# Kernel tuning notes

Hardware: AMD Instinct MI355X
Metric: run time of the kernel (lower is better)

The kernel has to match this reference:

```python
import jax, jax.numpy as jnp
import numpy as np

STRIDE = 4; R = 3; LEVELS = 4; LAT = 128; RES = (384, 512); D_IN = 1110; T_EMB = 50

def _sincos_1d(d, pos):
    omega = np.arange(d // 2, dtype=np.float64) / (d / 2.0)
    omega = 1.0 / 10000 ** omega
    out = pos.reshape(-1)[:, None] * omega[None, :]
    return np.concatenate([np.sin(out), np.cos(out)], axis=1).astype(np.float32)

def _support(coords, r):
    # coords [B, N, 3] (t, x, y) -> [B, N, 2r+1, 2r+1, 3]; offsets only in x,y
    d = jnp.linspace(-r, r, 2 * r + 1, dtype=jnp.float32)
    g0, g1 = jnp.meshgrid(d, d, indexing='ij')
    delta = jnp.stack([jnp.zeros_like(g0), g0, g1], axis=-1)
    return coords[:, :, None, None, :] + delta[None, None]

def _trilinear(fmap, coords):
    # fmap [B, C, Dd, H, W]; coords [B, M, 3] = (t, x, y); border padding, align_corners=True
    B, C, Dd, H, W = fmap.shape
    t = jnp.clip(coords[..., 0], 0.0, Dd - 1)
    x = jnp.clip(coords[..., 1], 0.0, W - 1)
    y = jnp.clip(coords[..., 2], 0.0, H - 1)
    t0f = jnp.floor(t); x0f = jnp.floor(x); y0f = jnp.floor(y)
    wt = (t - t0f)[:, None, :]; wx = (x - x0f)[:, None, :]; wy = (y - y0f)[:, None, :]
    t0 = t0f.astype(jnp.int32); t1 = jnp.minimum(t0 + 1, Dd - 1)
    x0 = x0f.astype(jnp.int32); x1 = jnp.minimum(x0 + 1, W - 1)
    y0 = y0f.astype(jnp.int32); y1 = jnp.minimum(y0 + 1, H - 1)
    flat = fmap.reshape(B, C, Dd * H * W)
    def g(ti, yi, xi):
        idx = (ti * H + yi) * W + xi
        return jnp.take_along_axis(flat, idx[:, None, :], axis=2)  # [B, C, M]
    def bilin(ti):
        v00 = g(ti, y0, x0); v01 = g(ti, y0, x1); v10 = g(ti, y1, x0); v11 = g(ti, y1, x1)
        return (v00 * (1 - wy) * (1 - wx) + v01 * (1 - wy) * wx
                + v10 * wy * (1 - wx) + v11 * wy * wx)
    return bilin(t0) * (1 - wt) + bilin(t1) * wt

def _posenc(x, min_deg, max_deg):
    scales = 2.0 ** jnp.arange(min_deg, max_deg, dtype=jnp.float32)
    xb = (x[..., None, :] * scales[:, None]).reshape(x.shape[:-1] + (-1,))
    ff = jnp.sin(jnp.concatenate([xb, xb + 0.5 * jnp.pi], axis=-1))
    return jnp.concatenate([x, ff], axis=-1)

def _interp_time(emb, t):
    T0 = emb.shape[1]
    if t == T0:
        return emb
    sc = T0 / float(t)
    j = jnp.clip((jnp.arange(t, dtype=jnp.float32) + 0.5) * sc - 0.5, 0.0, T0 - 1)
    j0 = jnp.floor(j).astype(jnp.int32); j1 = jnp.minimum(j0 + 1, T0 - 1)
    w = (j - j0)[None, :, None]
    return emb[:, j0] * (1 - w) + emb[:, j1] * w

def setup_inputs():
    key = jax.random.key(0)
    ks = jax.random.split(key, 10)
    B, T, N, H, W = 1, 16, 128, RES[0], RES[1]
    video = jax.random.uniform(ks[0], (B, T, 3, H, W), jnp.float32) * 255.0
    fr = jax.random.randint(ks[1], (B, N), 0, T).astype(jnp.float32)
    cx = jax.random.uniform(ks[2], (B, N), jnp.float32) * (W - 1)
    cy = jax.random.uniform(ks[3], (B, N), jnp.float32) * (H - 1)
    queries = jnp.stack([fr, cx, cy], axis=-1)
    s = 0.02
    return {
        'video': video,
        'queries': queries,
        'fnet_w': jax.random.normal(ks[4], (LAT, 3, 4, 4), jnp.float32) * s,
        'fnet_b': jnp.zeros((LAT,), jnp.float32),
        'fc1_w': jax.random.normal(ks[5], (2401, 384), jnp.float32) * s,
        'fc1_b': jnp.zeros((384,), jnp.float32),
        'fc2_w': jax.random.normal(ks[6], (384, 256), jnp.float32) * s,
        'fc2_b': jnp.zeros((256,), jnp.float32),
        'up_w1': jax.random.normal(ks[7], (D_IN, 384), jnp.float32) * s,
        'up_b1': jnp.zeros((384,), jnp.float32),
        'up_w2': jax.random.normal(ks[8], (384, 4), jnp.float32) * s,
        'up_b2': jnp.zeros((4,), jnp.float32),
        'time_emb': jnp.asarray(_sincos_1d(D_IN, np.linspace(0, T_EMB - 1, T_EMB))[None]),
        'iters': 4,
    }

def reference(video, queries, fnet_w, fnet_b, fc1_w, fc1_b, fc2_w, fc2_b,
              up_w1, up_b1, up_w2, up_b2, time_emb, iters):
    B, T, C, H, W = video.shape
    N = queries.shape[1]
    video = 2.0 * (video / 255.0) - 1.0
    qf = queries[:, :, 0]            # queried frames (used as float t coordinate)
    qc = queries[..., 1:3] / STRIDE  # (x, y) in feature-map coords
    # --- encoder (stand-in conv), L2-normalize over channels ---
    f = jax.lax.conv_general_dilated(video.reshape(B * T, C, H, W), fnet_w,
                                     (STRIDE, STRIDE), 'VALID') + fnet_b[None, :, None, None]
    f = f / jnp.sqrt(jnp.maximum(jnp.sum(f * f, axis=1, keepdims=True), 1e-12))
    fmaps = f.reshape(B, T, LAT, H // STRIDE, W // STRIDE)
    # --- avg-pool pyramid ---
    pyr = [fmaps]
    for _ in range(LEVELS - 1):
        p = pyr[-1]
        pyr.append(p.reshape(B, T, LAT, p.shape[-2] // 2, 2, p.shape[-1] // 2, 2).mean(axis=(4, 6)))
    r = R; rr = 2 * r + 1
    # --- track support features per level: [B, N, rr, rr, LAT] ---
    tfs = []
    for i in range(LEVELS):
        sc = jnp.concatenate([qf[..., None], qc / (2.0 ** i)], axis=-1)  # [B,N,3]
        sp = _support(sc, r).reshape(B, N * rr * rr, 3)
        feat = _trilinear(pyr[i].transpose(0, 2, 1, 3, 4), sp)  # [B, LAT, N*rr*rr]
        tfs.append(feat.reshape(B, LAT, N, rr, rr).transpose(0, 2, 3, 4, 1))
    vis = jnp.zeros((B, T, N), jnp.float32)
    conf = jnp.zeros((B, T, N), jnp.float32)
    coords = jnp.broadcast_to(qc.reshape(B, 1, N, 2), (B, T, N, 2)).astype(jnp.float32)
    scale = jnp.array([RES[1], RES[0]], jnp.float32) / STRIDE
    te = _interp_time(time_emb, T)  # [1, T, D_IN]
    for _ in range(iters):
        coords = jax.lax.stop_gradient(coords)
        cflat = coords.reshape(B * T, N, 2)
        embs = []
        for i in range(LEVELS):
            fm = pyr[i]
            Hi, Wi = fm.shape[-2], fm.shape[-1]
            sc = jnp.concatenate([jnp.zeros_like(cflat[..., :1]), cflat / (2.0 ** i)], axis=-1)
            sp = _support(sc, r).reshape(B * T, N * rr * rr, 3)
            cf = _trilinear(fm.reshape(B * T, LAT, 1, Hi, Wi), sp)  # [B*T, LAT, N*rr*rr]
            cf = cf.reshape(B, T, LAT, N, rr, rr).transpose(0, 1, 3, 4, 5, 2)  # [B,T,N,rr,rr,LAT]
            cv = jnp.einsum('btnhwc,bnijc->btnhwij', cf, tfs[i]).reshape(B * T * N, rr * rr * rr * rr)
            e = jax.nn.gelu(cv @ fc1_w + fc1_b, approximate=False) @ fc2_w + fc2_b
            embs.append(e)
        corr = jnp.concatenate(embs, axis=-1).reshape(B, T, N, -1)  # [B,T,N,1024]
        rf = jnp.pad(coords[:, :-1] - coords[:, 1:], ((0, 0), (0, 1), (0, 0), (0, 0))) / scale
        rb = jnp.pad(coords[:, 1:] - coords[:, :-1], ((0, 0), (1, 0), (0, 0), (0, 0))) / scale
        pe = _posenc(jnp.concatenate([rf, rb], axis=-1), 0, 10)  # [B,T,N,84]
        x = jnp.concatenate([vis[..., None], conf[..., None], corr, pe], axis=-1)  # [B,T,N,1110]
        x = x.transpose(0, 2, 1, 3) + te[None]  # [B,N,T,1110]
        delta = jax.nn.gelu(x @ up_w1 + up_b1, approximate=False) @ up_w2 + up_b2  # [B,N,T,4]
        coords = coords + delta[..., :2].transpose(0, 2, 1, 3)
        vis = vis + delta[..., 2].transpose(0, 2, 1)
        conf = conf + delta[..., 3].transpose(0, 2, 1)
    return coords * float(STRIDE), jax.nn.sigmoid(vis), jax.nn.sigmoid(conf)
```

## Files before the change

### kernel.cpp

```cpp
#include <hip/hip_runtime.h>
#include <math.h>

#define T_FR   16
#define N_Q    128
#define NSUP   49
#define H0     96
#define W0     128
#define DIN    1110
#define ITERS  4
#define KCV    2560
#define KU     1152

typedef __attribute__((ext_vector_type(8))) short short8;
typedef __attribute__((ext_vector_type(4))) float f32x4;

__device__ __forceinline__ float geluf(float x) {
    return 0.5f * x * (1.0f + erff(x * 0.70710678118654752f));
}
__device__ __forceinline__ unsigned short f2bf(float f) {
    unsigned u = __float_as_uint(f);
    u += 0x7fff + ((u >> 16) & 1);
    return (unsigned short)(u >> 16);
}
__device__ __forceinline__ float bf2f(unsigned short s) {
    return __uint_as_float(((unsigned)s) << 16);
}
__device__ __forceinline__ void async16(const void* g, void* l) {
    __builtin_amdgcn_global_load_lds(
        (const __attribute__((address_space(1))) void*)g,
        (__attribute__((address_space(3))) void*)l, 16, 0, 0);
}

__global__ void k_te(const float* __restrict__ emb, float* __restrict__ te) {
    int i = blockIdx.x * 256 + threadIdx.x;
    if (i >= T_FR * DIN) return;
    int t = i / DIN, d = i - t * DIN;
    float j = ((float)t + 0.5f) * (50.0f / 16.0f) - 0.5f;
    j = fminf(fmaxf(j, 0.0f), 49.0f);
    float j0f = floorf(j);
    int j0 = (int)j0f;
    int j1 = min(j0 + 1, 49);
    float w = j - j0f;
    te[i] = emb[j0 * DIN + d] * (1.0f - w) + emb[j1 * DIN + d] * w;
}

__global__ void k_init(const float* __restrict__ q, float* __restrict__ coords,
                       float* __restrict__ vis, float* __restrict__ conf) {
    int r = blockIdx.x * 256 + threadIdx.x;
    if (r >= T_FR * N_Q) return;
    int n = r & 127;
    coords[r * 2 + 0] = q[n * 3 + 1] * 0.25f;
    coords[r * 2 + 1] = q[n * 3 + 2] * 0.25f;
    vis[r] = 0.0f;
    conf[r] = 0.0f;
}

__global__ void k_prep1(const float* __restrict__ w, unsigned short* __restrict__ wt) {
    int i = blockIdx.x * 256 + threadIdx.x;
    if (i >= 2401 * 384) return;
    int k = i / 384, n = i - k * 384;
    int p = k / 49, q = k - p * 49;
    wt[(size_t)n * KCV + q * 52 + p] = f2bf(w[i]);
}

__global__ void k_prep(const float* __restrict__ w, unsigned short* __restrict__ wt,
                       int K, int N, int Ka, int total) {
    int i = blockIdx.x * 256 + threadIdx.x;
    if (i >= total) return;
    int k = i / N, n = i - k * N;
    wt[(size_t)n * Ka + k] = f2bf(w[i]);
}

__global__ void k_prepc(const float* __restrict__ w, unsigned short* __restrict__ wc) {
    int i = blockIdx.x * 256 + threadIdx.x;
    if (i >= 128 * 64) return;
    int ch = i >> 6, k = i & 63;
    wc[i] = (k < 48) ? f2bf(w[ch * 48 + k]) : (unsigned short)0;
}

#define APAD 72
__global__ __launch_bounds__(256) void k_conv(const float* __restrict__ video,
                                              const unsigned short* __restrict__ wc,
                                              const float* __restrict__ b,
                                              unsigned short* __restrict__ out) {
    __shared__ __align__(16) short As[128 * APAD];
    __shared__ __align__(16) short Bs[128 * APAD];
    const int y = blockIdx.x;
    const int tf = blockIdx.y;
    const int tid = threadIdx.x;

    {
        int pos = tid >> 1, half = tid & 1;
        short8 z = (short8){0,0,0,0,0,0,0,0};
        *(short8*)&As[pos * APAD + 48 + half * 8] = z;
    }
    #pragma unroll
    for (int s = 0; s < 6; ++s) {
        int chunk = s * 256 + tid;
        int c = chunk >> 9, r = chunk & 511;
        int ky = r >> 7, pos = r & 127;
        float4 v = *(const float4*)&video[(((size_t)(tf * 3 + c) * 384) + 4 * y + ky) * 512 + pos * 4];
        unsigned short o[4];
        o[0] = f2bf(v.x * (2.0f / 255.0f) - 1.0f);
        o[1] = f2bf(v.y * (2.0f / 255.0f) - 1.0f);
        o[2] = f2bf(v.z * (2.0f / 255.0f) - 1.0f);
        o[3] = f2bf(v.w * (2.0f / 255.0f) - 1.0f);
        *(uint2*)&As[pos * APAD + c * 16 + ky * 4] = *(const uint2*)o;
    }
    #pragma unroll
    for (int s = 0; s < 4; ++s) {
        int chunk = s * 256 + tid;
        int row = chunk >> 3, q = chunk & 7;
        *(uint4*)&Bs[row * APAD + q * 8] = *(const uint4*)&wc[row * 64 + q * 8];
    }
    __syncthreads();

    const int w = tid >> 6, lane = tid & 63, ml = lane & 15, quad = lane >> 4;
    f32x4 acc[2][8];
    #pragma unroll
    for (int mi = 0; mi < 2; ++mi)
        #pragma unroll
        for (int ni = 0; ni < 8; ++ni) acc[mi][ni] = (f32x4){0.f, 0.f, 0.f, 0.f};
    #pragma unroll
    for (int kk = 0; kk < 2; ++kk) {
        short8 af[2];
        #pragma unroll
        for (int mi = 0; mi < 2; ++mi)
            af[mi] = *(const short8*)&As[(w * 32 + mi * 16 + ml) * APAD + kk * 32 + quad * 8];
        #pragma unroll
        for (int ni = 0; ni < 8; ++ni) {
            short8 bv = *(const short8*)&Bs[(ni * 16 + ml) * APAD + kk * 32 + quad * 8];
            #pragma unroll
            for (int mi = 0; mi < 2; ++mi)
                acc[mi][ni] = __builtin_amdgcn_mfma_f32_16x16x32_bf16(af[mi], bv, acc[mi][ni], 0, 0, 0);
        }
    }
    float bias[8];
    #pragma unroll
    for (int ni = 0; ni < 8; ++ni) bias[ni] = b[ni * 16 + ml];
    unsigned short* obase = out + ((size_t)(tf * 96 + y) * 128) * 128;
    #pragma unroll
    for (int mi = 0; mi < 2; ++mi) {
        float s2[4];
        #pragma unroll
        for (int reg = 0; reg < 4; ++reg) {
            float s = 0.f;
            #pragma unroll
            for (int ni = 0; ni < 8; ++ni) {
                float v = acc[mi][ni][reg] + bias[ni];
                s = fmaf(v, v, s);
            }
            s += __shfl_xor(s, 1); s += __shfl_xor(s, 2);
            s += __shfl_xor(s, 4); s += __shfl_xor(s, 8);
            s2[reg] = rsqrtf(fmaxf(s, 1e-12f));
        }
        #pragma unroll
        for (int reg = 0; reg < 4; ++reg) {
            int pos = w * 32 + mi * 16 + quad * 4 + reg;
            #pragma unroll
            for (int ni = 0; ni < 8; ++ni)
                obase[(size_t)pos * 128 + ni * 16 + ml] = f2bf((acc[mi][ni][reg] + bias[ni]) * s2[reg]);
        }
    }
}

__global__ void k_pool(const unsigned short* __restrict__ in, unsigned short* __restrict__ out,
                       int Ho, int Wo, int total8) {
    int i = blockIdx.x * 256 + threadIdx.x;
    if (i >= total8) return;
    int c8 = i & 15;
    int rest = i >> 4;
    int x = rest % Wo; rest /= Wo;
    int y = rest % Ho;
    int bt = rest / Ho;
    int Wi = Wo * 2;
    const unsigned short* base = in + (size_t)bt * (Ho * 2) * Wi * 128;
    const unsigned short* p00 = base + ((size_t)(2 * y) * Wi + 2 * x) * 128 + c8 * 8;
    const unsigned short* p10 = base + ((size_t)(2 * y + 1) * Wi + 2 * x) * 128 + c8 * 8;
    unsigned short o[8];
    #pragma unroll
    for (int k = 0; k < 8; ++k)
        o[k] = f2bf(0.25f * (bf2f(p00[k]) + bf2f(p00[128 + k]) + bf2f(p10[k]) + bf2f(p10[128 + k])));
    unsigned short* dst = out + (size_t)i * 8;
    *(uint4*)dst = *(const uint4*)o;
}

__global__ __launch_bounds__(256) void k_template(const float* __restrict__ q,
    const unsigned short* __restrict__ p0, const unsigned short* __restrict__ p1,
    const unsigned short* __restrict__ p2, const unsigned short* __restrict__ p3,
    unsigned short* __restrict__ tfs) {
    __shared__ float gw[NSUP * 4];
    __shared__ int go[NSUP * 4];
    const int lvl = blockIdx.x >> 7;
    const int n = blockIdx.x & 127;
    const int tid = threadIdx.x;
    const unsigned short* fm; int Hi, Wi;
    if (lvl == 0)      { fm = p0; Hi = 96; Wi = 128; }
    else if (lvl == 1) { fm = p1; Hi = 48; Wi = 64; }
    else if (lvl == 2) { fm = p2; Hi = 24; Wi = 32; }
    else               { fm = p3; Hi = 12; Wi = 16; }
    float t = fminf(fmaxf(q[n * 3 + 0], 0.0f), (float)(T_FR - 1));
    float t0f = floorf(t);
    float wt = t - t0f;
    int t0 = (int)t0f, t1 = min(t0 + 1, T_FR - 1);
    if (tid < NSUP) {
        float inv = 1.0f / (float)(1 << lvl);
        float x = fminf(fmaxf(q[n * 3 + 1] * 0.25f * inv + (float)(tid / 7 - 3), 0.0f), (float)(Wi - 1));
        float y = fminf(fmaxf(q[n * 3 + 2] * 0.25f * inv + (float)(tid % 7 - 3), 0.0f), (float)(Hi - 1));
        float x0f = floorf(x), y0f = floorf(y);
        float wx = x - x0f, wy = y - y0f;
        int x0 = (int)x0f, y0 = (int)y0f;
        int x1 = min(x0 + 1, Wi - 1), y1 = min(y0 + 1, Hi - 1);
        gw[tid * 4 + 0] = (1 - wy) * (1 - wx);
        gw[tid * 4 + 1] = (1 - wy) * wx;
        gw[tid * 4 + 2] = wy * (1 - wx);
        gw[tid * 4 + 3] = wy * wx;
        go[tid * 4 + 0] = (y0 * Wi + x0) * 128;
        go[tid * 4 + 1] = (y0 * Wi + x1) * 128;
        go[tid * 4 + 2] = (y1 * Wi + x0) * 128;
        go[tid * 4 + 3] = (y1 * Wi + x1) * 128;
    }
    __syncthreads();
    size_t fs = (size_t)Hi * Wi * 128;
    const unsigned short* f0 = fm + (size_t)t0 * fs;
    const unsigned short* f1 = fm + (size_t)t1 * fs;
    unsigned short* obase = tfs + ((size_t)lvl * N_Q + n) * 64 * 128;
    #pragma unroll
    for (int s = 0; s < 4; ++s) {
        int i = s * 256 + tid;
        int p = i >> 4, c8 = i & 15;
        unsigned short o[8];
        if (p >= NSUP) {
            uint4 z = {0, 0, 0, 0};
            *(uint4*)&obase[(size_t)p * 128 + c8 * 8] = z;
            continue;
        }
        int o0 = go[p * 4 + 0] + c8 * 8, o1 = go[p * 4 + 1] + c8 * 8;
        int o2 = go[p * 4 + 2] + c8 * 8, o3 = go[p * 4 + 3] + c8 * 8;
        float w0 = gw[p * 4 + 0], w1 = gw[p * 4 + 1], w2 = gw[p * 4 + 2], w3 = gw[p * 4 + 3];
        uint4 a0 = *(const uint4*)&f0[o0], a1 = *(const uint4*)&f0[o1];
        uint4 a2 = *(const uint4*)&f0[o2], a3 = *(const uint4*)&f0[o3];
        uint4 b0 = *(const uint4*)&f1[o0], b1 = *(const uint4*)&f1[o1];
        uint4 b2 = *(const uint4*)&f1[o2], b3 = *(const uint4*)&f1[o3];
        const unsigned short* s0 = (const unsigned short*)&a0;
        const unsigned short* s1 = (const unsigned short*)&a1;
        const unsigned short* s2 = (const unsigned short*)&a2;
        const unsigned short* s3 = (const unsigned short*)&a3;
        const unsigned short* r0 = (const unsigned short*)&b0;
        const unsigned short* r1 = (const unsigned short*)&b1;
        const unsigned short* r2 = (const unsigned short*)&b2;
        const unsigned short* r3 = (const unsigned short*)&b3;
        #pragma unroll
        for (int j = 0; j < 8; ++j) {
            float v0 = w0 * bf2f(s0[j]) + w1 * bf2f(s1[j]) + w2 * bf2f(s2[j]) + w3 * bf2f(s3[j]);
            float v1 = w0 * bf2f(r0[j]) + w1 * bf2f(r1[j]) + w2 * bf2f(r2[j]) + w3 * bf2f(r3[j]);
            o[j] = f2bf(v0 * (1 - wt) + v1 * wt);
        }
        *(uint4*)&obase[(size_t)p * 128 + c8 * 8] = *(const uint4*)o;
    }
}

#define CPAD 136
__global__ __launch_bounds__(256) void k_corr(
    const unsigned short* __restrict__ p0, const unsigned short* __restrict__ p1,
    const unsigned short* __restrict__ p2, const unsigned short* __restrict__ p3,
    const unsigned short* __restrict__ tfs, const float* __restrict__ coords,
    unsigned short* __restrict__ cv) {
    __shared__ __align__(16) short tf_s[64 * CPAD];
    __shared__ __align__(16) short cf_s[64 * CPAD];
    __shared__ float gw[NSUP * 4];
    __shared__ int go[NSUP * 4];
    const int id = blockIdx.x;
    const int xcd = id & 7;
    const int j = id >> 3;
    const int lvl = j >> 8;
    const int bt = ((j >> 7) & 1) * 8 + xcd;
    const int n = j & 127;
    const int r = lvl * 2048 + bt * 128 + n;
    const int tid = threadIdx.x;

    const unsigned short* tsrc = tfs + ((size_t)lvl * N_Q + n) * 64 * 128;
    #pragma unroll
    for (int s = 0; s < 4; ++s) {
        int ch = s * 256 + tid;
        int row = ch >> 4, c8 = ch & 15;
        *(uint4*)&tf_s[row * CPAD + c8 * 8] = *(const uint4*)&tsrc[row * 128 + c8 * 8];
    }
    if (tid < 240) {
        int row = NSUP + tid / 16, c8 = tid % 16;
        uint4 z = {0, 0, 0, 0};
        *(uint4*)&cf_s[row * CPAD + c8 * 8] = z;
    }

    const unsigned short* fm; int Hi, Wi;
    if (lvl == 0)      { fm = p0; Hi = 96; Wi = 128; }
    else if (lvl == 1) { fm = p1; Hi = 48; Wi = 64; }
    else if (lvl == 2) { fm = p2; Hi = 24; Wi = 32; }
    else               { fm = p3; Hi = 12; Wi = 16; }
    if (tid < NSUP) {
        float inv = 1.0f / (float)(1 << lvl);
        float cx = coords[((size_t)bt * N_Q + n) * 2 + 0] * inv;
        float cy = coords[((size_t)bt * N_Q + n) * 2 + 1] * inv;
        float x = fminf(fmaxf(cx + (float)(tid / 7 - 3), 0.0f), (float)(Wi - 1));
        float y = fminf(fmaxf(cy + (float)(tid % 7 - 3), 0.0f), (float)(Hi - 1));
        float x0f = floorf(x), y0f = floorf(y);
        float wx = x - x0f, wy = y - y0f;
        int x0 = (int)x0f, y0 = (int)y0f;
        int x1 = min(x0 + 1, Wi - 1), y1 = min(y0 + 1, Hi - 1);
        gw[tid * 4 + 0] = (1 - wy) * (1 - wx);
        gw[tid * 4 + 1] = (1 - wy) * wx;
        gw[tid * 4 + 2] = wy * (1 - wx);
        gw[tid * 4 + 3] = wy * wx;
        go[tid * 4 + 0] = (y0 * Wi + x0) * 128;
        go[tid * 4 + 1] = (y0 * Wi + x1) * 128;
        go[tid * 4 + 2] = (y1 * Wi + x0) * 128;
        go[tid * 4 + 3] = (y1 * Wi + x1) * 128;
    }
    __syncthreads();

    const unsigned short* fbase = fm + (size_t)bt * Hi * Wi * 128;
    for (int i = tid; i < NSUP * 16; i += 256) {
        int p = i >> 4, c8 = i & 15;
        int o0 = go[p * 4 + 0] + c8 * 8, o1 = go[p * 4 + 1] + c8 * 8;
        int o2 = go[p * 4 + 2] + c8 * 8, o3 = go[p * 4 + 3] + c8 * 8;
        float w0 = gw[p * 4 + 0], w1 = gw[p * 4 + 1], w2 = gw[p * 4 + 2], w3 = gw[p * 4 + 3];
        uint4 a0 = *(const uint4*)&fbase[o0], a1 = *(const uint4*)&fbase[o1];
        uint4 a2 = *(const uint4*)&fbase[o2], a3 = *(const uint4*)&fbase[o3];
        const unsigned short* s0 = (const unsigned short*)&a0;
        const unsigned short* s1 = (const unsigned short*)&a1;
        const unsigned short* s2 = (const unsigned short*)&a2;
        const unsigned short* s3 = (const unsigned short*)&a3;
        unsigned short o[8];
        #pragma unroll
        for (int jj = 0; jj < 8; ++jj)
            o[jj] = f2bf(w0 * bf2f(s0[jj]) + w1 * bf2f(s1[jj]) + w2 * bf2f(s2[jj]) + w3 * bf2f(s3[jj]));
        *(uint4*)&cf_s[p * CPAD + c8 * 8] = *(const uint4*)o;
    }
    __syncthreads();

    const int w = tid >> 6, lane = tid & 63, ml = lane & 15, quad = lane >> 4;
    f32x4 acc[4];
    #pragma unroll
    for (int ni = 0; ni < 4; ++ni) acc[ni] = (f32x4){0.f, 0.f, 0.f, 0.f};
    #pragma unroll
    for (int kk = 0; kk < 4; ++kk) {
        short8 a = *(const short8*)&cf_s[(w * 16 + ml) * CPAD + kk * 32 + quad * 8];
        #pragma unroll
        for (int ni = 0; ni < 4; ++ni) {
            short8 b = *(const short8*)&tf_s[(ni * 16 + ml) * CPAD + kk * 32 + quad * 8];
            acc[ni] = __builtin_amdgcn_mfma_f32_16x16x32_bf16(a, b, acc[ni], 0, 0, 0);
        }
    }
    unsigned short* crow = cv + (size_t)r * KCV;
    const int p_base = w * 16 + quad * 4;
    #pragma unroll
    for (int ni = 0; ni < 4; ++ni) {
        int q = ni * 16 + ml;
        if (q < NSUP && p_base < 52) {
            unsigned short o4[4];
            #pragma unroll
            for (int reg = 0; reg < 4; ++reg) o4[reg] = f2bf(acc[ni][reg]);
            *(uint2*)&crow[q * 52 + p_base] = *(const uint2*)o4;
        }
    }
    if (tid < 12) crow[2548 + tid] = 0;
}

__global__ __launch_bounds__(256) void k_fc1(const unsigned short* __restrict__ A,
                                             const unsigned short* __restrict__ Wt,
                                             const float* __restrict__ bias,
                                             unsigned short* __restrict__ C,
                                             int Ka, int nbn, int nbm, int ldc) {
    __shared__ __align__(16) short As[64 * 32];
    __shared__ __align__(16) short Bs[128 * 32];
    const int id = blockIdx.x;
    const int xcd = id & 7;
    const int j = id >> 3;
    const int mpx = nbm >> 3;
    const int m_blk = xcd * mpx + j / nbn;
    const int n_blk = j % nbn;
    const int gm0 = m_blk * 64, n0 = n_blk * 128;
    const int tid = threadIdx.x;
    const int w = tid >> 6, lane = tid & 63, ml = lane & 15, quad = lane >> 4;
    const int wm = w >> 1, wn = w & 1;
    const int wbase = (tid & 192) * 16;
    f32x4 acc[2][4];
    #pragma unroll
    for (int mi = 0; mi < 2; ++mi)
        #pragma unroll
        for (int ni = 0; ni < 4; ++ni) acc[mi][ni] = (f32x4){0.f, 0.f, 0.f, 0.f};
    const unsigned short* gA = A + (size_t)(gm0 + (tid >> 2)) * Ka + (tid & 3) * 8;
    const unsigned short* gB = Wt + (size_t)n0 * Ka;
    for (int k0 = 0; k0 < Ka; k0 += 32) {
        async16(gA + k0, (char*)As + wbase);
        #pragma unroll
        for (int s = 0; s < 2; ++s) {
            int chunk = s * 256 + tid;
            int m = chunk >> 2, q = chunk & 3;
            async16(gB + (size_t)m * Ka + k0 + q * 8, (char*)Bs + s * 4096 + wbase);
        }
        __syncthreads();
        short8 af[2], bfr[4];
        #pragma unroll
        for (int mi = 0; mi < 2; ++mi)
            af[mi] = *(const short8*)&As[(wm * 32 + mi * 16 + ml) * 32 + quad * 8];
        #pragma unroll
        for (int ni = 0; ni < 4; ++ni)
            bfr[ni] = *(const short8*)&Bs[(wn * 64 + ni * 16 + ml) * 32 + quad * 8];
        #pragma unroll
        for (int mi = 0; mi < 2; ++mi)
            #pragma unroll
            for (int ni = 0; ni < 4; ++ni)
                acc[mi][ni] = __builtin_amdgcn_mfma_f32_16x16x32_bf16(af[mi], bfr[ni], acc[mi][ni], 0, 0, 0);
        __syncthreads();
    }
    #pragma unroll
    for (int mi = 0; mi < 2; ++mi) {
        #pragma unroll
        for (int ni = 0; ni < 4; ++ni) {
            int gn = n0 + wn * 64 + ni * 16 + ml;
            float bv = bias[gn];
            #pragma unroll
            for (int reg = 0; reg < 4; ++reg) {
                int gm = gm0 + wm * 32 + mi * 16 + quad * 4 + reg;
                C[(size_t)gm * ldc + gn] = f2bf(geluf(acc[mi][ni][reg] + bv));
            }
        }
    }
}

__global__ __launch_bounds__(256) void k_mgemm64(const unsigned short* __restrict__ A,
                                                 const unsigned short* __restrict__ Wt,
                                                 const float* __restrict__ bias,
                                                 void* __restrict__ Cout,
                                                 const float* __restrict__ te,
                                                 int Ka, int nbn, int nbm, int ldc, int mode) {
    __shared__ __align__(16) short As[64 * 64];
    __shared__ __align__(16) short Bs[64 * 64];
    const int id = blockIdx.x;
    const int xcd = id & 7;
    const int j = id >> 3;
    const int mpx = nbm >> 3;
    const int m_blk = xcd * mpx + j / nbn;
    const int n_blk = j % nbn;
    const int gm0 = m_blk * 64, n0 = n_blk * 64;
    const int tid = threadIdx.x;
    const int w = tid >> 6, lane = tid & 63, ml = lane & 15, quad = lane >> 4;
    const int wm = w >> 1, wn = w & 1;
    const int wbase = (tid & 192) * 16;
    const int srow = tid >> 3, sq = tid & 7;
    f32x4 acc[2][2];
    #pragma unroll
    for (int mi = 0; mi < 2; ++mi)
        #pragma unroll
        for (int ni = 0; ni < 2; ++ni) acc[mi][ni] = (f32x4){0.f, 0.f, 0.f, 0.f};
    const unsigned short* gA = A + (size_t)(gm0 + srow) * Ka + sq * 8;
    const unsigned short* gB = Wt + (size_t)(n0 + srow) * Ka + sq * 8;
    for (int k0 = 0; k0 < Ka; k0 += 64) {
        async16(gA + k0,           (char*)As + wbase);
        async16(gA + 32 * Ka + k0, (char*)As + 4096 + wbase);
        async16(gB + k0,           (char*)Bs + wbase);
        async16(gB + 32 * Ka + k0, (char*)Bs + 4096 + wbase);
        __syncthreads();
        #pragma unroll
        for (int kk = 0; kk < 2; ++kk) {
            short8 af[2], bfr[2];
            #pragma unroll
            for (int mi = 0; mi < 2; ++mi)
                af[mi] = *(const short8*)&As[(wm * 32 + mi * 16 + ml) * 64 + kk * 32 + quad * 8];
            #pragma unroll
            for (int ni = 0; ni < 2; ++ni)
                bfr[ni] = *(const short8*)&Bs[(wn * 32 + ni * 16 + ml) * 64 + kk * 32 + quad * 8];
            #pragma unroll
            for (int mi = 0; mi < 2; ++mi)
                #pragma unroll
                for (int ni = 0; ni < 2; ++ni)
                    acc[mi][ni] = __builtin_amdgcn_mfma_f32_16x16x32_bf16(af[mi], bfr[ni], acc[mi][ni], 0, 0, 0);
        }
        __syncthreads();
    }
    #pragma unroll
    for (int mi = 0; mi < 2; ++mi) {
        #pragma unroll
        for (int ni = 0; ni < 2; ++ni) {
            int gn = n0 + wn * 32 + ni * 16 + ml;
            float bv = bias[gn];
            #pragma unroll
            for (int reg = 0; reg < 4; ++reg) {
                int gm = gm0 + wm * 32 + mi * 16 + quad * 4 + reg;
                float v = acc[mi][ni][reg] + bv;
                if (mode == 1) v = geluf(v);
                if (mode == 2) {
                    int row = gm & 2047, lvl = gm >> 11;
                    int d = 2 + lvl * 256 + gn;
                    int t = row >> 7;
                    ((unsigned short*)Cout)[(size_t)row * KU + d] = f2bf(v + te[t * DIN + d]);
                } else {
                    ((unsigned short*)Cout)[(size_t)gm * ldc + gn] = f2bf(v);
                }
            }
        }
    }
}

__global__ __launch_bounds__(128) void k_assemble(const float* __restrict__ coords,
                           const float* __restrict__ vis, const float* __restrict__ conf,
                           const float* __restrict__ te, unsigned short* __restrict__ x) {
    int r = blockIdx.x;
    int tid = threadIdx.x;
    int d = (tid < 2) ? tid : 1024 + tid;
    int t = r >> 7, n = r & 127;
    if (d >= DIN) { x[(size_t)r * KU + d] = 0; return; }
    float v;
    if (d == 0) v = vis[r];
    else if (d == 1) v = conf[r];
    else {
        int dd = d - 1026;
        float c0x = coords[r * 2], c0y = coords[r * 2 + 1];
        float v4[4];
        if (t < T_FR - 1) {
            v4[0] = (c0x - coords[((t + 1) * N_Q + n) * 2 + 0]) * (1.0f / 128.0f);
            v4[1] = (c0y - coords[((t + 1) * N_Q + n) * 2 + 1]) * (1.0f / 96.0f);
        } else { v4[0] = 0.f; v4[1] = 0.f; }
        if (t > 0) {
            v4[2] = (c0x - coords[((t - 1) * N_Q + n) * 2 + 0]) * (1.0f / 128.0f);
            v4[3] = (c0y - coords[((t - 1) * N_Q + n) * 2 + 1]) * (1.0f / 96.0f);
        } else { v4[2] = 0.f; v4[3] = 0.f; }
        if (dd < 4) v = v4[dd];
        else if (dd < 44) { int s = (dd - 4) >> 2, k = (dd - 4) & 3; v = sinf(v4[k] * (float)(1 << s)); }
        else              { int s = (dd - 44) >> 2, k = (dd - 44) & 3; v = cosf(v4[k] * (float)(1 << s)); }
    }
    x[(size_t)r * KU + d] = f2bf(v + te[t * DIN + d]);
}

__global__ __launch_bounds__(256) void k_up2(const unsigned short* __restrict__ h1,
                                             const float* __restrict__ w2,
                                             const float* __restrict__ b2,
                                             float* __restrict__ coords,
                                             float* __restrict__ vis,
                                             float* __restrict__ conf) {
    const int w = threadIdx.x >> 6, lane = threadIdx.x & 63;
    const int r = blockIdx.x * 4 + w;
    float a0 = 0.f, a1 = 0.f, a2 = 0.f, a3 = 0.f;
    if (lane < 48) {
        short8 av = *(const short8*)&h1[(size_t)r * 384 + lane * 8];
        const float* wp = w2 + lane * 32;
        #pragma unroll
        for (int j = 0; j < 8; ++j) {
            float x = bf2f((unsigned short)av[j]);
            a0 = fmaf(x, wp[j * 4 + 0], a0);
            a1 = fmaf(x, wp[j * 4 + 1], a1);
            a2 = fmaf(x, wp[j * 4 + 2], a2);
            a3 = fmaf(x, wp[j * 4 + 3], a3);
        }
    }
    #pragma unroll
    for (int m = 32; m > 0; m >>= 1) {
        a0 += __shfl_xor(a0, m); a1 += __shfl_xor(a1, m);
        a2 += __shfl_xor(a2, m); a3 += __shfl_xor(a3, m);
    }
    if (lane == 0) {
        coords[r * 2 + 0] += a0 + b2[0];
        coords[r * 2 + 1] += a1 + b2[1];
        vis[r] += a2 + b2[2];
        conf[r] += a3 + b2[3];
    }
}

__global__ void k_output(const float* __restrict__ coords, const float* __restrict__ vis,
                         const float* __restrict__ conf, float* __restrict__ out) {
    int r = blockIdx.x * 256 + threadIdx.x;
    if (r >= T_FR * N_Q) return;
    out[r * 2 + 0] = coords[r * 2 + 0] * 4.0f;
    out[r * 2 + 1] = coords[r * 2 + 1] * 4.0f;
    out[4096 + r] = 1.0f / (1.0f + expf(-vis[r]));
    out[6144 + r] = 1.0f / (1.0f + expf(-conf[r]));
}

extern "C" void kernel_launch(void* const* d_in, const int* in_sizes, int n_in,
                              void* d_out, int out_size, void* d_ws, size_t ws_size,
                              hipStream_t stream) {
    const float* video   = (const float*)d_in[0];
    const float* queries = (const float*)d_in[1];
    const float* fnet_w  = (const float*)d_in[2];
    const float* fnet_b  = (const float*)d_in[3];
    const float* fc1_w   = (const float*)d_in[4];
    const float* fc1_b   = (const float*)d_in[5];
    const float* fc2_w   = (const float*)d_in[6];
    const float* fc2_b   = (const float*)d_in[7];
    const float* up_w1   = (const float*)d_in[8];
    const float* up_b1   = (const float*)d_in[9];
    const float* up_w2   = (const float*)d_in[10];
    const float* up_b2   = (const float*)d_in[11];
    const float* t_emb   = (const float*)d_in[12];

    char* wsb = (char*)d_ws;
    size_t off = 0;
    #define ALLOC_US(name, elems) unsigned short* name = (unsigned short*)(wsb + off); off += ((size_t)(elems) * 2 + 15) & ~15ull;
    #define ALLOC_F(name, elems)  float* name = (float*)(wsb + off); off += ((size_t)(elems) * 4 + 15) & ~15ull;
    ALLOC_US(pyr0, (size_t)16 * 96 * 128 * 128)
    ALLOC_US(pyr1, (size_t)16 * 48 * 64 * 128)
    ALLOC_US(pyr2, (size_t)16 * 24 * 32 * 128)
    ALLOC_US(pyr3, (size_t)16 * 12 * 16 * 128)
    ALLOC_US(tfs,  (size_t)4 * N_Q * 64 * 128)
    ALLOC_US(cv,   (size_t)8192 * KCV)
    ALLOC_US(h1,   (size_t)8192 * 384)
    ALLOC_US(xb,   (size_t)2048 * KU)
    ALLOC_US(wt1,  (size_t)384 * KCV)
    ALLOC_US(wt2,  (size_t)256 * 384)
    ALLOC_US(wtu,  (size_t)384 * KU)
    ALLOC_US(wcv,  (size_t)128 * 64)
    ALLOC_F(te,   (size_t)T_FR * DIN)
    ALLOC_F(crd,  (size_t)2048 * 2)
    ALLOC_F(vis,  2048)
    ALLOC_F(conf, 2048)

    k_te<<<(T_FR * DIN + 255) / 256, 256, 0, stream>>>(t_emb, te);
    k_init<<<8, 256, 0, stream>>>(queries, crd, vis, conf);
    hipMemsetAsync(wt1, 0, (size_t)384 * KCV * 2, stream);
    k_prep1<<<(2401 * 384 + 255) / 256, 256, 0, stream>>>(fc1_w, wt1);
    k_prep<<<(384 * 256 + 255) / 256, 256, 0, stream>>>(fc2_w, wt2, 384, 256, 384, 384 * 256);
    k_prep<<<(DIN * 384 + 255) / 256, 256, 0, stream>>>(up_w1, wtu, DIN, 384, KU, DIN * 384);
    k_prepc<<<32, 256, 0, stream>>>(fnet_w, wcv);
    k_conv<<<dim3(96, 16), 256, 0, stream>>>(video, wcv, fnet_b, pyr0);
    k_pool<<<(16 * 48 * 64 * 16 + 255) / 256, 256, 0, stream>>>(pyr0, pyr1, 48, 64, 16 * 48 * 64 * 16);
    k_pool<<<(16 * 24 * 32 * 16 + 255) / 256, 256, 0, stream>>>(pyr1, pyr2, 24, 32, 16 * 24 * 32 * 16);
    k_pool<<<(16 * 12 * 16 * 16 + 255) / 256, 256, 0, stream>>>(pyr2, pyr3, 12, 16, 16 * 12 * 16 * 16);
    k_template<<<4 * N_Q, 256, 0, stream>>>(queries, pyr0, pyr1, pyr2, pyr3, tfs);

    for (int it = 0; it < ITERS; ++it) {
        k_corr<<<8192, 256, 0, stream>>>(pyr0, pyr1, pyr2, pyr3, tfs, crd, cv);
        k_fc1<<<384, 256, 0, stream>>>(cv, wt1, fc1_b, h1, KCV, 3, 128, 384);
        k_assemble<<<2048, 128, 0, stream>>>(crd, vis, conf, te, xb);
        k_mgemm64<<<512, 256, 0, stream>>>(h1, wt2, fc2_b, xb, te, 384, 4, 128, 0, 2);
        k_mgemm64<<<192, 256, 0, stream>>>(xb, wtu, up_b1, h1, nullptr, KU, 6, 32, 384, 1);
        k_up2<<<512, 256, 0, stream>>>(h1, up_w2, up_b2, crd, vis, conf);
    }
    k_output<<<8, 256, 0, stream>>>(crd, vis, conf, (float*)d_out);
}
```

Before: 649.1 us.

## Replace LDS-staged GEMMs with register-prefetched direct-global-load MFMA kernel

Measured after the change: 930.5 us. 43.3% more time.

```diff
diff --git a/kernel.cpp b/kernel.cpp
--- a/kernel.cpp
+++ b/kernel.cpp
@@ -366,77 +366,12 @@
     if (tid < 12) crow[2548 + tid] = 0;
 }
 
-__global__ __launch_bounds__(256) void k_fc1(const unsigned short* __restrict__ A,
-                                             const unsigned short* __restrict__ Wt,
-                                             const float* __restrict__ bias,
-                                             unsigned short* __restrict__ C,
-                                             int Ka, int nbn, int nbm, int ldc) {
-    __shared__ __align__(16) short As[64 * 32];
-    __shared__ __align__(16) short Bs[128 * 32];
-    const int id = blockIdx.x;
-    const int xcd = id & 7;
-    const int j = id >> 3;
-    const int mpx = nbm >> 3;
-    const int m_blk = xcd * mpx + j / nbn;
-    const int n_blk = j % nbn;
-    const int gm0 = m_blk * 64, n0 = n_blk * 128;
-    const int tid = threadIdx.x;
-    const int w = tid >> 6, lane = tid & 63, ml = lane & 15, quad = lane >> 4;
-    const int wm = w >> 1, wn = w & 1;
-    const int wbase = (tid & 192) * 16;
-    f32x4 acc[2][4];
-    #pragma unroll
-    for (int mi = 0; mi < 2; ++mi)
-        #pragma unroll
-        for (int ni = 0; ni < 4; ++ni) acc[mi][ni] = (f32x4){0.f, 0.f, 0.f, 0.f};
-    const unsigned short* gA = A + (size_t)(gm0 + (tid >> 2)) * Ka + (tid & 3) * 8;
-    const unsigned short* gB = Wt + (size_t)n0 * Ka;
-    for (int k0 = 0; k0 < Ka; k0 += 32) {
-        async16(gA + k0, (char*)As + wbase);
-        #pragma unroll
-        for (int s = 0; s < 2; ++s) {
-            int chunk = s * 256 + tid;
-            int m = chunk >> 2, q = chunk & 3;
-            async16(gB + (size_t)m * Ka + k0 + q * 8, (char*)Bs + s * 4096 + wbase);
-        }
-        __syncthreads();
-        short8 af[2], bfr[4];
-        #pragma unroll
-        for (int mi = 0; mi < 2; ++mi)
-            af[mi] = *(const short8*)&As[(wm * 32 + mi * 16 + ml) * 32 + quad * 8];
-        #pragma unroll
-        for (int ni = 0; ni < 4; ++ni)
-            bfr[ni] = *(const short8*)&Bs[(wn * 64 + ni * 16 + ml) * 32 + quad * 8];
-        #pragma unroll
-        for (int mi = 0; mi < 2; ++mi)
-            #pragma unroll
-            for (int ni = 0; ni < 4; ++ni)
-                acc[mi][ni] = __builtin_amdgcn_mfma_f32_16x16x32_bf16(af[mi], bfr[ni], acc[mi][ni], 0, 0, 0);
-        __syncthreads();
-    }
-    #pragma unroll
-    for (int mi = 0; mi < 2; ++mi) {
-        #pragma unroll
-        for (int ni = 0; ni < 4; ++ni) {
-            int gn = n0 + wn * 64 + ni * 16 + ml;
-            float bv = bias[gn];
-            #pragma unroll
-            for (int reg = 0; reg < 4; ++reg) {
-                int gm = gm0 + wm * 32 + mi * 16 + quad * 4 + reg;
-                C[(size_t)gm * ldc + gn] = f2bf(geluf(acc[mi][ni][reg] + bv));
-            }
-        }
-    }
-}
-
-__global__ __launch_bounds__(256) void k_mgemm64(const unsigned short* __restrict__ A,
-                                                 const unsigned short* __restrict__ Wt,
-                                                 const float* __restrict__ bias,
-                                                 void* __restrict__ Cout,
-                                                 const float* __restrict__ te,
-                                                 int Ka, int nbn, int nbm, int ldc, int mode) {
-    __shared__ __align__(16) short As[64 * 64];
-    __shared__ __align__(16) short Bs[64 * 64];
+__global__ __launch_bounds__(256) void k_greg(const unsigned short* __restrict__ A,
+                                              const unsigned short* __restrict__ Wt,
+                                              const float* __restrict__ bias,
+                                              void* __restrict__ Cout,
+                                              const float* __restrict__ te,
+                                              int Ka, int nbn, int nbm, int ldc, int mode) {
     const int id = blockIdx.x;
     const int xcd = id & 7;
     const int j = id >> 3;
@@ -447,38 +382,56 @@
     const int tid = threadIdx.x;
     const int w = tid >> 6, lane = tid & 63, ml = lane & 15, quad = lane >> 4;
     const int wm = w >> 1, wn = w & 1;
-    const int wbase = (tid & 192) * 16;
-    const int srow = tid >> 3, sq = tid & 7;
+
     f32x4 acc[2][2];
     #pragma unroll
     for (int mi = 0; mi < 2; ++mi)
         #pragma unroll
         for (int ni = 0; ni < 2; ++ni) acc[mi][ni] = (f32x4){0.f, 0.f, 0.f, 0.f};
-    const unsigned short* gA = A + (size_t)(gm0 + srow) * Ka + sq * 8;
-    const unsigned short* gB = Wt + (size_t)(n0 + srow) * Ka + sq * 8;
-    for (int k0 = 0; k0 < Ka; k0 += 64) {
-        async16(gA + k0,           (char*)As + wbase);
-        async16(gA + 32 * Ka + k0, (char*)As + 4096 + wbase);
-        async16(gB + k0,           (char*)Bs + wbase);
-        async16(gB + 32 * Ka + k0, (char*)Bs + 4096 + wbase);
-        __syncthreads();
+
+    const unsigned short* pa0 = A + (size_t)(gm0 + wm * 32 + ml) * Ka + quad * 8;
+    const unsigned short* pa1 = pa0 + (size_t)16 * Ka;
+    const unsigned short* pb0 = Wt + (size_t)(n0 + wn * 32 + ml) * Ka + quad * 8;
+    const unsigned short* pb1 = pb0 + (size_t)16 * Ka;
+
+    short8 a0[2][2], b0[2][2];
+    #pragma unroll
+    for (int kk = 0; kk < 2; ++kk) {
+        a0[0][kk] = *(const short8*)(pa0 + kk * 32);
+        a0[1][kk] = *(const short8*)(pa1 + kk * 32);
+        b0[0][kk] = *(const short8*)(pb0 + kk * 32);
+        b0[1][kk] = *(const short8*)(pb1 + kk * 32);
+    }
+    for (int k0 = 64; k0 < Ka; k0 += 64) {
+        short8 a1[2][2], b1[2][2];
         #pragma unroll
         for (int kk = 0; kk < 2; ++kk) {
-            short8 af[2], bfr[2];
-            #pragma unroll
-            for (int mi = 0; mi < 2; ++mi)
-                af[mi] = *(const short8*)&As[(wm * 32 + mi * 16 + ml) * 64 + kk * 32 + quad * 8];
-            #pragma unroll
-            for (int ni = 0; ni < 2; ++ni)
-                bfr[ni] = *(const short8*)&Bs[(wn * 32 + ni * 16 + ml) * 64 + kk * 32 + quad * 8];
+            a1[0][kk] = *(const short8*)(pa0 + k0 + kk * 32);
+            a1[1][kk] = *(const short8*)(pa1 + k0 + kk * 32);
+            b1[0][kk] = *(const short8*)(pb0 + k0 + kk * 32);
+            b1[1][kk] = *(const short8*)(pb1 + k0 + kk * 32);
+        }
+        #pragma unroll
+        for (int kk = 0; kk < 2; ++kk)
             #pragma unroll
             for (int mi = 0; mi < 2; ++mi)
                 #pragma unroll
                 for (int ni = 0; ni < 2; ++ni)
-                    acc[mi][ni] = __builtin_amdgcn_mfma_f32_16x16x32_bf16(af[mi], bfr[ni], acc[mi][ni], 0, 0, 0);
-        }
-        __syncthreads();
-    }
+                    acc[mi][ni] = __builtin_amdgcn_mfma_f32_16x16x32_bf16(a0[mi][kk], b0[ni][kk], acc[mi][ni], 0, 0, 0);
+        #pragma unroll
+        for (int kk = 0; kk < 2; ++kk) {
+            a0[0][kk] = a1[0][kk]; a0[1][kk] = a1[1][kk];
+            b0[0][kk] = b1[0][kk]; b0[1][kk] = b1[1][kk];
+        }
+    }
+    #pragma unroll
+    for (int kk = 0; kk < 2; ++kk)
+        #pragma unroll
+        for (int mi = 0; mi < 2; ++mi)
+            #pragma unroll
+            for (int ni = 0; ni < 2; ++ni)
+                acc[mi][ni] = __builtin_amdgcn_mfma_f32_16x16x32_bf16(a0[mi][kk], b0[ni][kk], acc[mi][ni], 0, 0, 0);
+
     #pragma unroll
     for (int mi = 0; mi < 2; ++mi) {
         #pragma unroll
@@ -630,10 +583,10 @@
 
     for (int it = 0; it < ITERS; ++it) {
         k_corr<<<8192, 256, 0, stream>>>(pyr0, pyr1, pyr2, pyr3, tfs, crd, cv);
-        k_fc1<<<384, 256, 0, stream>>>(cv, wt1, fc1_b, h1, KCV, 3, 128, 384);
+        k_greg<<<768, 256, 0, stream>>>(cv, wt1, fc1_b, h1, nullptr, KCV, 6, 128, 384, 1);
         k_assemble<<<2048, 128, 0, stream>>>(crd, vis, conf, te, xb);
-        k_mgemm64<<<512, 256, 0, stream>>>(h1, wt2, fc2_b, xb, te, 384, 4, 128, 0, 2);
-        k_mgemm64<<<192, 256, 0, stream>>>(xb, wtu, up_b1, h1, nullptr, KU, 6, 32, 384, 1);
+        k_greg<<<512, 256, 0, stream>>>(h1, wt2, fc2_b, xb, te, 384, 4, 128, 0, 2);
+        k_greg<<<192, 256, 0, stream>>>(xb, wtu, up_b1, h1, nullptr, KU, 6, 32, 384, 1);
         k_up2<<<512, 256, 0, stream>>>(h1, up_w2, up_b2, crd, vis, conf);
     }
     k_output<<<8, 256, 0, stream>>>(crd, vis, conf, (float*)d_out);
```

## Split-K the fc1 and update-MLP GEMMs with a separate bias+GELU reduction

Applied to the files above, without the earlier changes.

Result: faster. 626.3 us (-3.5%).

```diff
diff --git a/kernel.cpp b/kernel.cpp
--- a/kernel.cpp
+++ b/kernel.cpp
@@ -366,77 +366,14 @@
     if (tid < 12) crow[2548 + tid] = 0;
 }
 
-__global__ __launch_bounds__(256) void k_fc1(const unsigned short* __restrict__ A,
-                                             const unsigned short* __restrict__ Wt,
-                                             const float* __restrict__ bias,
-                                             unsigned short* __restrict__ C,
-                                             int Ka, int nbn, int nbm, int ldc) {
+__global__ __launch_bounds__(256) void k_mg(const unsigned short* __restrict__ A,
+                                            const unsigned short* __restrict__ Wt,
+                                            const float* __restrict__ bias,
+                                            void* __restrict__ Cout,
+                                            const float* __restrict__ te,
+                                            int Ka, int nbn, int nbm, int ldc, int mode) {
     __shared__ __align__(16) short As[64 * 32];
-    __shared__ __align__(16) short Bs[128 * 32];
-    const int id = blockIdx.x;
-    const int xcd = id & 7;
-    const int j = id >> 3;
-    const int mpx = nbm >> 3;
-    const int m_blk = xcd * mpx + j / nbn;
-    const int n_blk = j % nbn;
-    const int gm0 = m_blk * 64, n0 = n_blk * 128;
-    const int tid = threadIdx.x;
-    const int w = tid >> 6, lane = tid & 63, ml = lane & 15, quad = lane >> 4;
-    const int wm = w >> 1, wn = w & 1;
-    const int wbase = (tid & 192) * 16;
-    f32x4 acc[2][4];
-    #pragma unroll
-    for (int mi = 0; mi < 2; ++mi)
-        #pragma unroll
-        for (int ni = 0; ni < 4; ++ni) acc[mi][ni] = (f32x4){0.f, 0.f, 0.f, 0.f};
-    const unsigned short* gA = A + (size_t)(gm0 + (tid >> 2)) * Ka + (tid & 3) * 8;
-    const unsigned short* gB = Wt + (size_t)n0 * Ka;
-    for (int k0 = 0; k0 < Ka; k0 += 32) {
-        async16(gA + k0, (char*)As + wbase);
-        #pragma unroll
-        for (int s = 0; s < 2; ++s) {
-            int chunk = s * 256 + tid;
-            int m = chunk >> 2, q = chunk & 3;
-            async16(gB + (size_t)m * Ka + k0 + q * 8, (char*)Bs + s * 4096 + wbase);
-        }
-        __syncthreads();
-        short8 af[2], bfr[4];
-        #pragma unroll
-        for (int mi = 0; mi < 2; ++mi)
-            af[mi] = *(const short8*)&As[(wm * 32 + mi * 16 + ml) * 32 + quad * 8];
-        #pragma unroll
-        for (int ni = 0; ni < 4; ++ni)
-            bfr[ni] = *(const short8*)&Bs[(wn * 64 + ni * 16 + ml) * 32 + quad * 8];
-        #pragma unroll
-        for (int mi = 0; mi < 2; ++mi)
-            #pragma unroll
-            for (int ni = 0; ni < 4; ++ni)
-                acc[mi][ni] = __builtin_amdgcn_mfma_f32_16x16x32_bf16(af[mi], bfr[ni], acc[mi][ni], 0, 0, 0);
-        __syncthreads();
-    }
-    #pragma unroll
-    for (int mi = 0; mi < 2; ++mi) {
-        #pragma unroll
-        for (int ni = 0; ni < 4; ++ni) {
-            int gn = n0 + wn * 64 + ni * 16 + ml;
-            float bv = bias[gn];
-            #pragma unroll
-            for (int reg = 0; reg < 4; ++reg) {
-                int gm = gm0 + wm * 32 + mi * 16 + quad * 4 + reg;
-                C[(size_t)gm * ldc + gn] = f2bf(geluf(acc[mi][ni][reg] + bv));
-            }
-        }
-    }
-}
-
-__global__ __launch_bounds__(256) void k_mgemm64(const unsigned short* __restrict__ A,
-                                                 const unsigned short* __restrict__ Wt,
-                                                 const float* __restrict__ bias,
-                                                 void* __restrict__ Cout,
-                                                 const float* __restrict__ te,
-                                                 int Ka, int nbn, int nbm, int ldc, int mode) {
-    __shared__ __align__(16) short As[64 * 64];
-    __shared__ __align__(16) short Bs[64 * 64];
+    __shared__ __align__(16) short Bs[64 * 32];
     const int id = blockIdx.x;
     const int xcd = id & 7;
     const int j = id >> 3;
@@ -448,35 +385,30 @@
     const int w = tid >> 6, lane = tid & 63, ml = lane & 15, quad = lane >> 4;
     const int wm = w >> 1, wn = w & 1;
     const int wbase = (tid & 192) * 16;
-    const int srow = tid >> 3, sq = tid & 7;
+    const int sm = tid >> 2, sq = tid & 3;
     f32x4 acc[2][2];
     #pragma unroll
     for (int mi = 0; mi < 2; ++mi)
         #pragma unroll
         for (int ni = 0; ni < 2; ++ni) acc[mi][ni] = (f32x4){0.f, 0.f, 0.f, 0.f};
-    const unsigned short* gA = A + (size_t)(gm0 + srow) * Ka + sq * 8;
-    const unsigned short* gB = Wt + (size_t)(n0 + srow) * Ka + sq * 8;
-    for (int k0 = 0; k0 < Ka; k0 += 64) {
-        async16(gA + k0,           (char*)As + wbase);
-        async16(gA + 32 * Ka + k0, (char*)As + 4096 + wbase);
-        async16(gB + k0,           (char*)Bs + wbase);
-        async16(gB + 32 * Ka + k0, (char*)Bs + 4096 + wbase);
+    const unsigned short* gA = A + (size_t)(gm0 + sm) * Ka + sq * 8;
+    const unsigned short* gB = Wt + (size_t)(n0 + sm) * Ka + sq * 8;
+    for (int k0 = 0; k0 < Ka; k0 += 32) {
+        async16(gA + k0, (char*)As + wbase);
+        async16(gB + k0, (char*)Bs + wbase);
         __syncthreads();
-        #pragma unroll
-        for (int kk = 0; kk < 2; ++kk) {
-            short8 af[2], bfr[2];
-            #pragma unroll
-            for (int mi = 0; mi < 2; ++mi)
-                af[mi] = *(const short8*)&As[(wm * 32 + mi * 16 + ml) * 64 + kk * 32 + quad * 8];
+        short8 af[2], bfr[2];
+        #pragma unroll
+        for (int mi = 0; mi < 2; ++mi)
+            af[mi] = *(const short8*)&As[(wm * 32 + mi * 16 + ml) * 32 + quad * 8];
+        #pragma unroll
+        for (int ni = 0; ni < 2; ++ni)
+            bfr[ni] = *(const short8*)&Bs[(wn * 32 + ni * 16 + ml) * 32 + quad * 8];
+        #pragma unroll
+        for (int mi = 0; mi < 2; ++mi)
             #pragma unroll
             for (int ni = 0; ni < 2; ++ni)
-                bfr[ni] = *(const short8*)&Bs[(wn * 32 + ni * 16 + ml) * 64 + kk * 32 + quad * 8];
-            #pragma unroll
-            for (int mi = 0; mi < 2; ++mi)
-                #pragma unroll
-                for (int ni = 0; ni < 2; ++ni)
-                    acc[mi][ni] = __builtin_amdgcn_mfma_f32_16x16x32_bf16(af[mi], bfr[ni], acc[mi][ni], 0, 0, 0);
-        }
+                acc[mi][ni] = __builtin_amdgcn_mfma_f32_16x16x32_bf16(af[mi], bfr[ni], acc[mi][ni], 0, 0, 0);
         __syncthreads();
     }
     #pragma unroll
@@ -501,6 +433,89 @@
             }
         }
     }
+}
+
+__global__ __launch_bounds__(256) void k_ms(const unsigned short* __restrict__ A,
+                                            const unsigned short* __restrict__ Wt,
+                                            float* __restrict__ Pbase,
+                                            int Ka, int nbn, int nbm, int N,
+                                            int nsteps, int S, int M) {
+    __shared__ __align__(16) short As[64 * 32];
+    __shared__ __align__(16) short Bs[64 * 32];
+    const int id = blockIdx.x;
+    const int xcd = id & 7;
+    const int j = id >> 3;
+    const int mpx = nbm >> 3;
+    const int sS = j % S;
+    const int jj = j / S;
+    const int m_blk = xcd * mpx + jj / nbn;
+    const int n_blk = jj % nbn;
+    const int gm0 = m_blk * 64, n0 = n_blk * 64;
+    const int kb = sS * (nsteps / S), ke = kb + nsteps / S;
+    const int tid = threadIdx.x;
+    const int w = tid >> 6, lane = tid & 63, ml = lane & 15, quad = lane >> 4;
+    const int wm = w >> 1, wn = w & 1;
+    const int wbase = (tid & 192) * 16;
+    const int sm = tid >> 2, sq = tid & 3;
+    f32x4 acc[2][2];
+    #pragma unroll
+    for (int mi = 0; mi < 2; ++mi)
+        #pragma unroll
+        for (int ni = 0; ni < 2; ++ni) acc[mi][ni] = (f32x4){0.f, 0.f, 0.f, 0.f};
+    const unsigned short* gA = A + (size_t)(gm0 + sm) * Ka + sq * 8;
+    const unsigned short* gB = Wt + (size_t)(n0 + sm) * Ka + sq * 8;
+    for (int k0 = kb * 32; k0 < ke * 32; k0 += 32) {
+        async16(gA + k0, (char*)As + wbase);
+        async16(gB + k0, (char*)Bs + wbase);
+        __syncthreads();
+        short8 af[2], bfr[2];
+        #pragma unroll
+        for (int mi = 0; mi < 2; ++mi)
+            af[mi] = *(const short8*)&As[(wm * 32 + mi * 16 + ml) * 32 + quad * 8];
+        #pragma unroll
+        for (int ni = 0; ni < 2; ++ni)
+            bfr[ni] = *(const short8*)&Bs[(wn * 32 + ni * 16 + ml) * 32 + quad * 8];
+        #pragma unroll
+        for (int mi = 0; mi < 2; ++mi)
+            #pragma unroll
+            for (int ni = 0; ni < 2; ++ni)
+                acc[mi][ni] = __builtin_amdgcn_mfma_f32_16x16x32_bf16(af[mi], bfr[ni], acc[mi][ni], 0, 0, 0);
+        __syncthreads();
+    }
+    float* P = Pbase + (size_t)sS * M * N;
+    #pragma unroll
+    for (int mi = 0; mi < 2; ++mi) {
+        #pragma unroll
+        for (int ni = 0; ni < 2; ++ni) {
+            int gn = n0 + wn * 32 + ni * 16 + ml;
+            #pragma unroll
+            for (int reg = 0; reg < 4; ++reg) {
+                int gm = gm0 + wm * 32 + mi * 16 + quad * 4 + reg;
+                P[(size_t)gm * N + gn] = acc[mi][ni][reg];
+            }
+        }
+    }
+}
+
+__global__ __launch_bounds__(256) void k_red(const float* __restrict__ P,
+                                             const float* __restrict__ bias,
+                                             unsigned short* __restrict__ out,
+                                             int MN4, int N4, int S) {
+    int i4 = blockIdx.x * 256 + threadIdx.x;
+    if (i4 >= MN4) return;
+    const float4* Pv = (const float4*)P;
+    float4 v = Pv[i4];
+    for (int s = 1; s < S; ++s) {
+        float4 u = Pv[(size_t)s * MN4 + i4];
+        v.x += u.x; v.y += u.y; v.z += u.z; v.w += u.w;
+    }
+    const float4 b = *(const float4*)&bias[(i4 % N4) * 4];
+    unsigned short o[4];
+    o[0] = f2bf(geluf(v.x + b.x));
+    o[1] = f2bf(geluf(v.y + b.y));
+    o[2] = f2bf(geluf(v.z + b.z));
+    o[3] = f2bf(geluf(v.w + b.w));
+    *(uint2*)&out[(size_t)i4 * 4] = *(const uint2*)o;
 }
 
 __global__ __launch_bounds__(128) void k_assemble(const float* __restrict__ coords,
@@ -610,6 +625,7 @@
     ALLOC_US(wt2,  (size_t)256 * 384)
     ALLOC_US(wtu,  (size_t)384 * KU)
     ALLOC_US(wcv,  (size_t)128 * 64)
+    ALLOC_F(pp,   (size_t)2 * 8192 * 384)
     ALLOC_F(te,   (size_t)T_FR * DIN)
     ALLOC_F(crd,  (size_t)2048 * 2)
     ALLOC_F(vis,  2048)
@@ -630,10 +646,12 @@
 
     for (int it = 0; it < ITERS; ++it) {
         k_corr<<<8192, 256, 0, stream>>>(pyr0, pyr1, pyr2, pyr3, tfs, crd, cv);
-        k_fc1<<<384, 256, 0, stream>>>(cv, wt1, fc1_b, h1, KCV, 3, 128, 384);
+        k_ms<<<1536, 256, 0, stream>>>(cv, wt1, pp, KCV, 6, 128, 384, 80, 2, 8192);
+        k_red<<<3072, 256, 0, stream>>>(pp, fc1_b, h1, 8192 * 96, 96, 2);
         k_assemble<<<2048, 128, 0, stream>>>(crd, vis, conf, te, xb);
-        k_mgemm64<<<512, 256, 0, stream>>>(h1, wt2, fc2_b, xb, te, 384, 4, 128, 0, 2);
-        k_mgemm64<<<192, 256, 0, stream>>>(xb, wtu, up_b1, h1, nullptr, KU, 6, 32, 384, 1);
+        k_mg<<<512, 256, 0, stream>>>(h1, wt2, fc2_b, xb, te, 384, 4, 128, 0, 2);
+        k_ms<<<768, 256, 0, stream>>>(xb, wtu, pp, KU, 6, 32, 384, 36, 4, 2048);
+        k_red<<<768, 256, 0, stream>>>(pp, up_b1, h1, 2048 * 96, 96, 4);
         k_up2<<<512, 256, 0, stream>>>(h1, up_w2, up_b2, crd, vis, conf);
     }
     k_output<<<8, 256, 0, stream>>>(crd, vis, conf, (float*)d_out);
```
